# Kernel tuning notes

Measured on AMD Instinct MI355X. Metric: run time of the kernel, lower is better.

## Reference

```python
import jax, jax.numpy as jnp
import numpy as np

B, N, D, H = 8, 4096, 256, 4
KP, KN = N // 16, N // 32
EPS = 1e-6

def _ln(x, g, b):
    m = jnp.mean(x, -1, keepdims=True)
    v = jnp.var(x, -1, keepdims=True)
    return (x - m) / jnp.sqrt(v + 1e-5) * g + b

def _cross_attn(q_in, kv_in, wq, wk, wv, wo, bo):
    # q_in [1,Nq,D], kv_in [1,Nk,D]
    Bq, Nq, Dm = q_in.shape
    Nk = kv_in.shape[1]
    dh = Dm // H
    q = (q_in @ wq).reshape(Bq, Nq, H, dh).transpose(0, 2, 1, 3)
    k = (kv_in @ wk).reshape(Bq, Nk, H, dh).transpose(0, 2, 1, 3)
    v = (kv_in @ wv).reshape(Bq, Nk, H, dh).transpose(0, 2, 1, 3)
    attn = jax.nn.softmax(jnp.einsum('bhqd,bhkd->bhqk', q, k) * (dh ** -0.5), axis=-1)
    out = jnp.einsum('bhqk,bhkd->bhqd', attn, v).transpose(0, 2, 1, 3).reshape(Bq, Nq, Dm)
    return out @ wo + bo

def setup_inputs():
    key = jax.random.key(0)
    ks = jax.random.split(key, 40)
    f32 = jnp.float32
    def w(i, shape, s):
        return s * jax.random.normal(ks[i], shape, f32)
    inp = {}
    inp['x'] = jax.random.normal(ks[0], (B, N, D), f32)
    inp['mask'] = (jax.random.randint(ks[1], (B, N), 0, 3) - 1).astype(jnp.int32)  # values in {-1,0,1}
    inp['pos_emb'] = 0.02 * jax.random.normal(ks[2], (1, N, D), f32)
    inp['sim_p_w'] = w(3, (D, D), 0.2); inp['sim_p_b'] = jnp.zeros((D,), f32)
    inp['sim_n_w'] = w(4, (D, D), 0.2); inp['sim_n_b'] = jnp.zeros((D,), f32)
    inp['adj_w'] = w(5, (D, D), 0.05)
    inp['gnn_p_w1'] = w(6, (D, D), 0.05); inp['gnn_p_w2'] = w(7, (D, D), 0.05)
    inp['gnn_n_w1'] = w(8, (D, D), 0.05); inp['gnn_n_w2'] = w(9, (D, D), 0.05)
    for i in range(1, 6):
        inp['ln%d_g' % i] = jnp.ones((D,), f32)
        inp['ln%d_b' % i] = jnp.zeros((D,), f32)
    names = ['i2q_wq', 'i2q_wk', 'i2q_wv', 'i2q_wo', 'q2i_wq', 'q2i_wk', 'q2i_wv', 'q2i_wo']
    for j, nme in enumerate(names):
        inp[nme] = w(10 + j, (D, D), 0.05)
    inp['i2q_bo'] = jnp.zeros((D,), f32)
    inp['q2i_bo'] = jnp.zeros((D,), f32)
    inp['mlp_w'] = w(20, (D, D), 0.05); inp['mlp_b'] = jnp.zeros((D,), f32)
    inp['g_i2t'] = 0.1 * jax.random.normal(ks[21], (1, 1, D), f32)
    inp['g_t2i'] = 0.1 * jax.random.normal(ks[22], (1, 1, D), f32)
    return inp

def reference(x, mask, pos_emb, sim_p_w, sim_p_b, sim_n_w, sim_n_b, adj_w,
              gnn_p_w1, gnn_p_w2, gnn_n_w1, gnn_n_w2,
              ln1_g, ln1_b, ln2_g, ln2_b, ln3_g, ln3_b, ln4_g, ln4_b, ln5_g, ln5_b,
              i2q_wq, i2q_wk, i2q_wv, i2q_wo, i2q_bo,
              q2i_wq, q2i_wk, q2i_wv, q2i_wo, q2i_bo,
              mlp_w, mlp_b, g_i2t, g_t2i):
    pos_mask = (mask == 1).astype(x.dtype)[..., None]    # [B,N,1]
    neg_mask = (mask == -1).astype(x.dtype)[..., None]
    pos_query = (x * pos_mask).sum(1, keepdims=True) / (pos_mask.sum(1, keepdims=True) + EPS)  # [B,1,D]
    neg_query = (x * neg_mask).sum(1, keepdims=True) / (neg_mask.sum(1, keepdims=True) + EPS)
    pos_sim = jax.nn.sigmoid(((x @ sim_p_w + sim_p_b) * pos_query).sum(-1))  # [B,N]
    neg_sim = jax.nn.sigmoid(((x @ sim_n_w + sim_n_b) * neg_query).sum(-1))
    weight_p, idx_p = jax.lax.top_k(pos_sim, KP)
    weight_n, idx_n = jax.lax.top_k(neg_sim, KN)
    scale = 1.0 / jnp.sqrt(jnp.asarray(D, x.dtype))

    def gcn(node, w1, w2):
        adj = jax.nn.softmax((node @ adj_w) @ node.T * scale, axis=-1)  # [K,K]
        h = jax.nn.relu(adj @ (node @ w1))
        return adj @ (h @ w2)

    def batch_forward(ip, wp, inn, wn, feat):
        node_p = feat[ip] * (wp > 0.6).astype(feat.dtype)[:, None]       # [KP,D]
        query_p = gcn(node_p, gnn_p_w1, gnn_p_w2) + pos_emb[0, ip]
        node_n = feat[inn] * (wn > 0.6).astype(feat.dtype)[:, None]      # [KN,D]
        query_n = gcn(node_n, gnn_n_w1, gnn_n_w2) + pos_emb[0, inn]
        query = jnp.concatenate([query_p, query_n], 0)[None]             # [1,KP+KN,D]
        featb = feat[None]                                               # [1,N,D]
        query = query + g_i2t * _cross_attn(_ln(query, ln1_g, ln1_b), _ln(featb, ln2_g, ln2_b),
                                            i2q_wq, i2q_wk, i2q_wv, i2q_wo, i2q_bo)
        featb = featb + g_t2i * _cross_attn(_ln(featb, ln3_g, ln3_b), _ln(query, ln4_g, ln4_b),
                                            q2i_wq, q2i_wk, q2i_wv, q2i_wo, q2i_bo)
        featb = featb + (_ln(featb, ln5_g, ln5_b) @ mlp_w + mlp_b)
        return featb

    out = jax.vmap(batch_forward)(idx_p, weight_p, idx_n, weight_n, x)   # [B,1,N,D]
    return out, pos_sim, neg_sim
```

## Files before the change

### kernel.cpp

```cpp
#include <hip/hip_runtime.h>

#define BB 8
#define NN 4096
#define DD 256
#define HH 4
#define DHH 64
#define KPP 256
#define KNN 128
#define SCH 64

typedef float f32x4 __attribute__((ext_vector_type(4)));
typedef short bf16x8 __attribute__((ext_vector_type(8)));
typedef short bf16x4 __attribute__((ext_vector_type(4)));

#define FLAG_TRANSB 1
#define FLAG_RELU   2

__device__ __forceinline__ float bf2f(unsigned short u){
  union { unsigned int i; float f; } v; v.i = ((unsigned int)u) << 16; return v.f;
}
__device__ __forceinline__ unsigned short f2bf(float f){
  union { float f; unsigned int i; } v; v.f = f;
  return (unsigned short)((v.i + 0x7FFFu + ((v.i >> 16) & 1u)) >> 16);
}
__device__ __forceinline__ void gload16(const void* g, void* l){
  __builtin_amdgcn_global_load_lds((const __attribute__((address_space(1))) void*)g,
                                   (__attribute__((address_space(3))) void*)l, 16, 0, 0);
}

__global__ __launch_bounds__(256) void stats_part(const float* __restrict__ x,
                                                  const int* __restrict__ mask,
                                                  float* __restrict__ part,
                                                  float* __restrict__ pcnt){
  int b = blockIdx.y, c = blockIdx.x, t = threadIdx.x;
  int w = t >> 6, lane = t & 63;
  const int R = NN / SCH;
  int n0 = c * R;
  const float* xb = x + ((long)b*NN + n0)*DD;
  const int* mb = mask + (long)b*NN + n0;
  float4 sp = {0.f,0.f,0.f,0.f}, sn = {0.f,0.f,0.f,0.f};
  int cp = 0, cn = 0;
  #pragma unroll 4
  for (int r = w; r < R; r += 4){
    int mv = mb[r];
    float4 v = ((const float4*)(xb + (long)r*DD))[lane];
    if (mv == 1){ sp.x += v.x; sp.y += v.y; sp.z += v.z; sp.w += v.w; cp++; }
    else if (mv == -1){ sn.x += v.x; sn.y += v.y; sn.z += v.z; sn.w += v.w; cn++; }
  }
  __shared__ float red[2][4][256];
  __shared__ int cnt[2][4];
  ((float4*)&red[0][w][0])[lane] = sp;
  ((float4*)&red[1][w][0])[lane] = sn;
  if (lane == 0){ cnt[0][w] = cp; cnt[1][w] = cn; }
  __syncthreads();
  float s0 = red[0][0][t]+red[0][1][t]+red[0][2][t]+red[0][3][t];
  float s1 = red[1][0][t]+red[1][1][t]+red[1][2][t]+red[1][3][t];
  part[(((long)(b*SCH+c)*2+0)*DD)+t] = s0;
  part[(((long)(b*SCH+c)*2+1)*DD)+t] = s1;
  if (t == 0){
    pcnt[(b*SCH+c)*2+0] = (float)(cnt[0][0]+cnt[0][1]+cnt[0][2]+cnt[0][3]);
    pcnt[(b*SCH+c)*2+1] = (float)(cnt[1][0]+cnt[1][1]+cnt[1][2]+cnt[1][3]);
  }
}

__global__ void stats_vec(const float* __restrict__ part, const float* __restrict__ pcnt,
                          const float* __restrict__ bp, const float* __restrict__ bn,
                          float* __restrict__ qpn, float* __restrict__ cscal){
  int b = blockIdx.x, k = threadIdx.x;
  __shared__ float red[256];
  float sp=0.f, sn=0.f, cp=0.f, cn=0.f;
  for (int c = 0; c < SCH; c++){
    sp += part[(((long)(b*SCH+c)*2+0)*DD)+k];
    sn += part[(((long)(b*SCH+c)*2+1)*DD)+k];
    cp += pcnt[(b*SCH+c)*2+0];
    cn += pcnt[(b*SCH+c)*2+1];
  }
  float qpv = sp / (cp + 1e-6f);
  float qnv = sn / (cn + 1e-6f);
  qpn[(long)(b*2+0)*DD + k] = qpv;
  qpn[(long)(b*2+1)*DD + k] = qnv;
  red[k] = bp[k]*qpv;
  __syncthreads();
  for (int s = 128; s > 0; s >>= 1){ if (k < s) red[k] += red[k+s]; __syncthreads(); }
  if (k == 0) cscal[b*2+0] = red[0];
  __syncthreads();
  red[k] = bn[k]*qnv;
  __syncthreads();
  for (int s = 128; s > 0; s >>= 1){ if (k < s) red[k] += red[k+s]; __syncthreads(); }
  if (k == 0) cscal[b*2+1] = red[0];
}

__global__ void simvec_par(const float* __restrict__ qpn,
                           const float* __restrict__ Wp, const float* __restrict__ Wn,
                           float* __restrict__ vvec){
  int c = blockIdx.x, b = blockIdx.y, t = threadIdx.x;
  __shared__ float qp[256], qn[256];
  qp[t] = qpn[(long)(b*2+0)*DD + t];
  qn[t] = qpn[(long)(b*2+1)*DD + t];
  __syncthreads();
  int row = c*32 + (t >> 3);
  int seg = (t & 7)*32;
  const float* wp = Wp + (long)row*DD + seg;
  const float* wn = Wn + (long)row*DD + seg;
  float ap = 0.f, an = 0.f;
  #pragma unroll 8
  for (int j = 0; j < 32; j++){ ap += wp[j]*qp[seg+j]; an += wn[j]*qn[seg+j]; }
  #pragma unroll
  for (int off = 1; off < 8; off <<= 1){ ap += __shfl_xor(ap, off); an += __shfl_xor(an, off); }
  if ((t & 7) == 0){
    vvec[(long)(b*2+0)*DD + row] = ap;
    vvec[(long)(b*2+1)*DD + row] = an;
  }
}

__global__ void sim_norm_kernel(const float* __restrict__ x, const float* __restrict__ vvec,
                                const float* __restrict__ cscal,
                                float* __restrict__ simP, float* __restrict__ simN,
                                unsigned short* __restrict__ xhat){
  int b = blockIdx.y;
  int w = threadIdx.x >> 6, lane = threadIdx.x & 63;
  int n = blockIdx.x*4 + w;
  long row = (long)b*NN + n;
  const float4* xr = (const float4*)(x + row*DD);
  float4 xv = xr[lane];
  float4 a = ((const float4*)(vvec + (long)(b*2+0)*DD))[lane];
  float4 c = ((const float4*)(vvec + (long)(b*2+1)*DD))[lane];
  float sp = xv.x*a.x + xv.y*a.y + xv.z*a.z + xv.w*a.w;
  float sn = xv.x*c.x + xv.y*c.y + xv.z*c.z + xv.w*c.w;
  float s  = xv.x+xv.y+xv.z+xv.w;
  float q  = xv.x*xv.x+xv.y*xv.y+xv.z*xv.z+xv.w*xv.w;
  for (int off = 32; off; off >>= 1){
    sp += __shfl_xor(sp, off); sn += __shfl_xor(sn, off);
    s  += __shfl_xor(s, off);  q  += __shfl_xor(q, off);
  }
  float m = s*(1.f/256.f);
  float var = q*(1.f/256.f) - m*m;
  float rinv = rsqrtf(var + 1e-5f);
  ushort4 o;
  o.x = f2bf((xv.x-m)*rinv); o.y = f2bf((xv.y-m)*rinv);
  o.z = f2bf((xv.z-m)*rinv); o.w = f2bf((xv.w-m)*rinv);
  ((ushort4*)(xhat + row*DD))[lane] = o;
  if (lane == 0){
    float zp = sp + cscal[b*2+0], zn = sn + cscal[b*2+1];
    simP[row] = 1.f/(1.f+expf(-zp));
    simN[row] = 1.f/(1.f+expf(-zn));
  }
}

__global__ __launch_bounds__(256) void topk_radix(const float* __restrict__ simP,
                                                  const float* __restrict__ simN,
                                                  const float* __restrict__ x,
                                                  int* __restrict__ idxb, float* __restrict__ wb,
                                                  float* __restrict__ node){
  __shared__ unsigned int vals[4096];
  __shared__ unsigned int hist[4096];
  __shared__ unsigned short eql[4096];
  __shared__ unsigned int tsum[256];
  __shared__ unsigned int sB, sRem, sCG, sCnt, sEq;
  int id = blockIdx.x; int sgn = id & 1, b = id >> 1;
  int K = (sgn == 0) ? KPP : KNN;
  const float* s = (sgn == 0 ? simP : simN) + (long)b*NN;
  int t = threadIdx.x;
  if (t == 0){ sCG = 0; sCnt = 0; sEq = 0; }
  for (int i = t; i < 4096; i += 256){ vals[i] = __float_as_uint(s[i]); hist[i] = 0; }
  __syncthreads();

  auto find_thresh = [&](int NB, unsigned need){
    int per = NB >> 8;
    int base = t*per;
    unsigned local = 0;
    for (int j = 0; j < per; j++) local += hist[base+j];
    tsum[t] = local;
    __syncthreads();
    #pragma unroll
    for (int st = 1; st < 256; st <<= 1){
      unsigned v = (t + st < 256) ? tsum[t+st] : 0u;
      __syncthreads();
      tsum[t] += v;
      __syncthreads();
    }
    unsigned after = (t < 255) ? tsum[t+1] : 0u;
    if (after < need && after + local >= need){
      unsigned c = after;
      for (int j = per-1; j >= 0; j--){
        unsigned h = hist[base+j];
        c += h;
        if (c >= need){
          sB = (unsigned)(base+j);
          sRem = need - (c - h);
          atomicAdd(&sCG, c - h);
          break;
        }
      }
    }
    __syncthreads();
  };

  for (int i = t; i < 4096; i += 256) atomicAdd(&hist[vals[i] >> 20], 1u);
  __syncthreads();
  find_thresh(4096, (unsigned)K);
  unsigned B1 = sB, rem1 = sRem;
  __syncthreads();
  for (int i = t; i < 4096; i += 256) hist[i] = 0;
  __syncthreads();
  for (int i = t; i < 4096; i += 256){
    unsigned v = vals[i];
    if ((v >> 20) == B1) atomicAdd(&hist[(v >> 8) & 0xFFFu], 1u);
  }
  __syncthreads();
  find_thresh(4096, rem1);
  unsigned B2 = sB, rem2 = sRem;
  unsigned pre = (B1 << 12) | B2;
  __syncthreads();
  hist[t] = 0;
  __syncthreads();
  for (int i = t; i < 4096; i += 256){
    unsigned v = vals[i];
    if ((v >> 8) == pre) atomicAdd(&hist[v & 0xFFu], 1u);
  }
  __syncthreads();
  find_thresh(256, rem2);
  unsigned T = (pre << 8) | sB;
  unsigned cg = sCG;
  __syncthreads();
  hist[t] = 0;
  __syncthreads();

  int* oi = idxb + (long)id*256;
  float* ow = wb + (long)id*256;
  for (int i = t; i < 4096; i += 256){
    unsigned v = vals[i];
    if (v > T){
      unsigned p = atomicAdd(&sCnt, 1u);
      oi[p] = i; ow[p] = __uint_as_float(v);
      hist[p] = (unsigned)i; hist[256+p] = v;
    }
    else if (v == T){ unsigned e = atomicAdd(&sEq, 1u); eql[e] = (unsigned short)i; }
  }
  __syncthreads();
  int ne = K - (int)cg;
  int eqn = (int)sEq;
  for (int e = t; e < eqn; e += 256){
    int myi = eql[e]; int r = 0;
    for (int e2 = 0; e2 < eqn; e2++) r += (eql[e2] < myi);
    if (r < ne){
      oi[cg + r] = myi; ow[cg + r] = __uint_as_float(T);
      hist[cg + r] = (unsigned)myi; hist[256 + cg + r] = T;
    }
  }
  __syncthreads();
  int rbase = (sgn == 0) ? 0 : KPP;
  int lane = t & 63, rw = t >> 6;
  for (int i0 = 0; i0 < K; i0 += 4){
    int r = i0 + rw;
    int idx = (int)hist[r];
    float wv = __uint_as_float(hist[256 + r]);
    float4 vsel;
    if (wv > 0.6f) vsel = ((const float4*)(x + ((long)b*NN + idx)*DD))[lane];
    else vsel = (float4){0.f,0.f,0.f,0.f};
    ((float4*)(node + ((long)b*384 + rbase + r)*DD))[lane] = vsel;
  }
}

__global__ void softmax_dual(float* __restrict__ A0, int L0, int rpb0, long bs0, int rows0,
                             float* __restrict__ A1, int L1, int rpb1, long bs1, int rows1){
  int w = threadIdx.x >> 6, lane = threadIdx.x & 63;
  long row = (long)blockIdx.x*4 + w;
  float* A; int L, rpb; long bs;
  if (row < rows0){ A = A0; L = L0; rpb = rpb0; bs = bs0; }
  else { row -= rows0; if (row >= rows1) return; A = A1; L = L1; rpb = rpb1; bs = bs1; }
  int b = (int)(row / rpb), r = (int)(row % rpb);
  float* a = A + (long)b*bs + (long)r*L;
  int e = L >> 6;
  float vals[4]; float mx = -1e30f;
  for (int j = 0; j < e; j++){ vals[j] = a[lane*e+j]; mx = fmaxf(mx, vals[j]); }
  for (int off = 32; off; off >>= 1) mx = fmaxf(mx, __shfl_xor(mx, off));
  float sum = 0.f;
  for (int j = 0; j < e; j++){ vals[j] = expf(vals[j]-mx); sum += vals[j]; }
  for (int off = 32; off; off >>= 1) sum += __shfl_xor(sum, off);
  float rinv = 1.f/sum;
  for (int j = 0; j < e; j++) a[lane*e+j] = vals[j]*rinv;
}

__global__ void rownorm_kernel(const float* __restrict__ X, unsigned short* __restrict__ Y, int rows){
  int w = threadIdx.x >> 6, lane = threadIdx.x & 63;
  long row = (long)blockIdx.x*4 + w;
  if (row >= rows) return;
  const float4* xr = (const float4*)(X + row*DD);
  float4 xv = xr[lane];
  float s = xv.x+xv.y+xv.z+xv.w;
  float q = xv.x*xv.x+xv.y*xv.y+xv.z*xv.z+xv.w*xv.w;
  for (int off = 32; off; off >>= 1){ s += __shfl_xor(s, off); q += __shfl_xor(q, off); }
  float m = s*(1.f/256.f);
  float var = q*(1.f/256.f) - m*m;
  float rinv = rsqrtf(var + 1e-5f);
  ushort4 o;
  o.x = f2bf((xv.x-m)*rinv); o.y = f2bf((xv.y-m)*rinv);
  o.z = f2bf((xv.z-m)*rinv); o.w = f2bf((xv.w-m)*rinv);
  ((ushort4*)(Y + row*DD))[lane] = o;
}

struct FoldArgs { const float* W[9]; const float* g[9]; unsigned short* BT[9]; float sc[9]; };
struct BiasArgs { const float* W[7]; const float* b[7]; const float* addb[7]; float* out[7]; float sc[7]; };

__global__ void fold_all(FoldArgs fa, BiasArgs ba){
  __shared__ float T[64][65];
  int t = threadIdx.x;
  if (blockIdx.y < 9){
    int m = blockIdx.y, tile = blockIdx.x;
    const float* W = fa.W[m]; const float* g = fa.g[m]; unsigned short* BT = fa.BT[m];
    float sc = fa.sc[m];
    int tn = (tile & 3)*64, tk = (tile >> 2)*64;
    #pragma unroll 4
    for (int p = 0; p < 16; p++){
      int kl = p*4 + (t >> 6), nl = t & 63;
      float v = W[(long)(tk+kl)*256 + tn + nl];
      if (g) v *= g[tk+kl];
      T[kl][nl] = v * sc;
    }
    __syncthreads();
    #pragma unroll 4
    for (int p = 0; p < 16; p++){
      int nl = p*4 + (t >> 6), kl = t & 63;
      BT[(long)(tn+nl)*256 + tk + kl] = f2bf(T[kl][nl]);
    }
  } else if (blockIdx.x < 7){
    int m = blockIdx.x, n = t;
    const float* W = ba.W[m]; const float* b = ba.b[m];
    float s = (ba.addb[m] != nullptr) ? ba.addb[m][n] : 0.f;
    for (int k = 0; k < 256; k++) s += b[k]*W[(long)k*256+n];
    ba.out[m][n] = s * ba.sc[m];
  }
}

struct GP {
  const float* A; long sAb; int lda;
  const float* B; long sBb; int ldb;
  float* C; long sCb; int ldc;
  const int* pidx; const float* pe;
  int M, N, K; float alpha; int flags;
};
struct GP4 { GP p[4]; };

__global__ __launch_bounds__(256) void gemm_multi(GP4 g4){
  GP p = g4.p[blockIdx.z >> 3];
  int b = blockIdx.z & 7;
  int m0 = blockIdx.y*64, n0 = blockIdx.x*64;
  if (m0 >= p.M || n0 >= p.N) return;
  __shared__ __align__(16) unsigned short As[64*40];
  __shared__ __align__(16) unsigned short Bs[64*40];
  const float* Ab = p.A + (long)b*p.sAb;
  const float* Bb = p.B + (long)b*p.sBb;
  int t = threadIdx.x;
  int w = t >> 6, lane = t & 63, lrowi = lane & 15, lquad = lane >> 4;
  int wm = w >> 1, wn = w & 1;
  f32x4 acc[2][2];
  #pragma unroll
  for (int i = 0; i < 2; i++)
    #pragma unroll
    for (int j = 0; j < 2; j++) acc[i][j] = (f32x4){0.f,0.f,0.f,0.f};
  int am = t >> 2, akq = t & 3;
  for (int k0 = 0; k0 < p.K; k0 += 32){
    {
      const float4* s4 = (const float4*)(Ab + (long)(m0+am)*p.lda + k0 + akq*8);
      float4 u = s4[0], vv = s4[1];
      unsigned short tmp[8];
      tmp[0]=f2bf(u.x); tmp[1]=f2bf(u.y); tmp[2]=f2bf(u.z); tmp[3]=f2bf(u.w);
      tmp[4]=f2bf(vv.x); tmp[5]=f2bf(vv.y); tmp[6]=f2bf(vv.z); tmp[7]=f2bf(vv.w);
      *(uint4*)(&As[am*40 + akq*8]) = *(uint4*)tmp;
    }
    if (p.flags & FLAG_TRANSB){
      const float4* s4 = (const float4*)(Bb + (long)(n0+am)*p.ldb + k0 + akq*8);
      float4 u = s4[0], vv = s4[1];
      unsigned short tmp[8];
      tmp[0]=f2bf(u.x); tmp[1]=f2bf(u.y); tmp[2]=f2bf(u.z); tmp[3]=f2bf(u.w);
      tmp[4]=f2bf(vv.x); tmp[5]=f2bf(vv.y); tmp[6]=f2bf(vv.z); tmp[7]=f2bf(vv.w);
      *(uint4*)(&Bs[am*40 + akq*8]) = *(uint4*)tmp;
    } else {
      int bn = t & 63, bkb = (t >> 6)*8;
      #pragma unroll
      for (int j = 0; j < 8; j++)
        Bs[bn*40 + bkb + j] = f2bf(Bb[(long)(k0+bkb+j)*p.ldb + n0 + bn]);
    }
    __syncthreads();
    bf16x8 af[2], bfr[2];
    #pragma unroll
    for (int i = 0; i < 2; i++)
      af[i] = *(const bf16x8*)(&As[(wm*32 + i*16 + lrowi)*40 + lquad*8]);
    #pragma unroll
    for (int j = 0; j < 2; j++)
      bfr[j] = *(const bf16x8*)(&Bs[(wn*32 + j*16 + lrowi)*40 + lquad*8]);
    #pragma unroll
    for (int i = 0; i < 2; i++)
      #pragma unroll
      for (int j = 0; j < 2; j++)
        acc[i][j] = __builtin_amdgcn_mfma_f32_16x16x32_bf16(af[i], bfr[j], acc[i][j], 0, 0, 0);
    __syncthreads();
  }
  float* Cb = p.C + (long)b*p.sCb;
  #pragma unroll
  for (int i = 0; i < 2; i++)
    #pragma unroll
    for (int j = 0; j < 2; j++){
      int col = n0 + wn*32 + j*16 + lrowi;
      #pragma unroll
      for (int r = 0; r < 4; r++){
        int row = m0 + wm*32 + i*16 + lquad*4 + r;
        float v = p.alpha*acc[i][j][r];
        if (p.flags & FLAG_RELU) v = fmaxf(v, 0.f);
        if (p.pidx != nullptr){
          int idx = p.pidx[b*512 + row];
          v += p.pe[(long)idx*256 + col];
        }
        Cb[(long)row*p.ldc + col] = v;
      }
    }
}

template<typename OT, bool RES, bool GATE>
__device__ __forceinline__ void gemm128_body(
    const unsigned short* __restrict__ A, long sAb,
    const unsigned short* __restrict__ BT,
    OT* __restrict__ C, long sCb, int ldc,
    const float* __restrict__ R, long sRb,
    const float* __restrict__ bias, const float* __restrict__ gate,
    int bx, int by, int bz,
    unsigned short (&As)[2][4096], unsigned short (&Bs)[2][4096])
{
  int t = threadIdx.x;
  int w = t >> 6, lane = t & 63, lrowi = lane & 15, lquad = lane >> 4;
  int wm = w >> 1, wn = w & 1;
  int m0 = by*128, n0 = bx*128;
  const unsigned short* Ab = A + (long)bz*sAb + (long)m0*256;
  const unsigned short* Bb = BT + (long)n0*256;
  int g0 = t, g1 = 256 + t;
  int row0 = g0 >> 2, kq0 = g0 & 3;
  int row1 = g1 >> 2, kq1 = g1 & 3;
  f32x4 acc[4][4];
  #pragma unroll
  for (int i = 0; i < 4; i++)
    #pragma unroll
    for (int j = 0; j < 4; j++) acc[i][j] = (f32x4){0.f,0.f,0.f,0.f};

  auto stage = [&](int buf, int k0){
    gload16(Ab + (long)row0*256 + k0 + kq0*8, &As[buf][g0*8]);
    gload16(Ab + (long)row1*256 + k0 + kq1*8, &As[buf][g1*8]);
    gload16(Bb + (long)row0*256 + k0 + kq0*8, &Bs[buf][g0*8]);
    gload16(Bb + (long)row1*256 + k0 + kq1*8, &Bs[buf][g1*8]);
  };

  stage(0, 0);
  for (int it = 0; it < 8; it++){
    int cur = it & 1;
    if (it < 7){
      stage(cur ^ 1, (it+1)*32);
      __asm__ volatile("s_waitcnt vmcnt(4)" ::: "memory");
    } else {
      __asm__ volatile("s_waitcnt vmcnt(0)" ::: "memory");
    }
    __builtin_amdgcn_s_barrier();
    bf16x8 af[4], bfr[4];
    #pragma unroll
    for (int i = 0; i < 4; i++)
      af[i] = *(const bf16x8*)(&As[cur][((wm*64 + i*16 + lrowi)*4 + lquad)*8]);
    #pragma unroll
    for (int j = 0; j < 4; j++)
      bfr[j] = *(const bf16x8*)(&Bs[cur][((wn*64 + j*16 + lrowi)*4 + lquad)*8]);
    #pragma unroll
    for (int i = 0; i < 4; i++)
      #pragma unroll
      for (int j = 0; j < 4; j++)
        acc[i][j] = __builtin_amdgcn_mfma_f32_16x16x32_bf16(af[i], bfr[j], acc[i][j], 0, 0, 0);
    __asm__ volatile("s_waitcnt lgkmcnt(0)" ::: "memory");
    __builtin_amdgcn_s_barrier();
  }
  OT* Cb = C + (long)bz*sCb;
  const float* Rb = RES ? (R + (long)bz*sRb) : nullptr;
  #pragma unroll
  for (int j = 0; j < 4; j++){
    int col = n0 + wn*64 + j*16 + lrowi;
    float bv = bias[col];
    float gv = GATE ? gate[col] : 1.f;
    #pragma unroll
    for (int i = 0; i < 4; i++){
      #pragma unroll
      for (int r = 0; r < 4; r++){
        int row = m0 + wm*64 + i*16 + lquad*4 + r;
        float v = acc[i][j][r] + bv;
        if (GATE) v *= gv;
        if (RES) v += Rb[(long)row*256 + col];
        if constexpr (sizeof(OT) == 4) Cb[(long)row*ldc + col] = v;
        else                           Cb[(long)row*ldc + col] = f2bf(v);
      }
    }
  }
}

template<typename OT, bool RES, bool GATE>
__global__ __launch_bounds__(256) void gemm128(
    const unsigned short* __restrict__ A, long sAb,
    const unsigned short* __restrict__ BT,
    OT* __restrict__ C, long sCb, int ldc,
    const float* __restrict__ R, long sRb,
    const float* __restrict__ bias, const float* __restrict__ gate)
{
  __shared__ __align__(16) unsigned short As[2][4096];
  __shared__ __align__(16) unsigned short Bs[2][4096];
  gemm128_body<OT,RES,GATE>(A, sAb, BT, C, sCb, ldc, R, sRb, bias, gate,
                            blockIdx.x, blockIdx.y, blockIdx.z, As, Bs);
}

__global__ __launch_bounds__(256) void gemm128_pair(
    const unsigned short* __restrict__ A0, long sA0, const unsigned short* __restrict__ B0,
    unsigned short* __restrict__ C0, long sC0, int ldc0, const float* __restrict__ bias0,
    const unsigned short* __restrict__ A1, long sA1, const unsigned short* __restrict__ B1,
    unsigned short* __restrict__ C1, long sC1, int ldc1, const float* __restrict__ bias1)
{
  __shared__ __align__(16) unsigned short As[2][4096];
  __shared__ __align__(16) unsigned short Bs[2][4096];
  int x = blockIdx.x, z = blockIdx.z;
  if (x < 192){
    gemm128_body<unsigned short,false,false>(A0, sA0, B0, C0, sC0, ldc0, nullptr, 0, bias0, nullptr,
                                             x % 6, x / 6, z, As, Bs);
  } else {
    int xx = x - 192;
    gemm128_body<unsigned short,false,false>(A1, sA1, B1, C1, sC1, ldc1, nullptr, 0, bias1, nullptr,
                                             xx % 2, xx / 2, z, As, Bs);
  }
}

template<int NFRAG>
__global__ __launch_bounds__(256) void flash_kernel(
    const unsigned short* __restrict__ Q, long sQb, int ldq,
    const unsigned short* __restrict__ Kt, const unsigned short* __restrict__ Vt,
    long sKb, int ldkv,
    unsigned short* __restrict__ O, long sOb,
    float* __restrict__ Opart, float* __restrict__ Lpart,
    int Nq, int Nk, int nsplit)
{
  __shared__ __align__(16) unsigned short Kl[2][32*72];
  __shared__ __align__(16) unsigned short Vl[2][64*36];
  __shared__ __align__(16) unsigned short Pl[4*NFRAG*16*36];
  int b = blockIdx.z, h = blockIdx.y;
  int nqg = Nq / (64*NFRAG);
  int qg = blockIdx.x % nqg, split = blockIdx.x / nqg;
  int kchunk = Nk / nsplit;
  int kbeg = split*kchunk, kend = kbeg + kchunk;
  int t = threadIdx.x, w = t >> 6, lane = t & 63, lrowi = lane & 15, lquad = lane >> 4;
  int q0 = qg*(64*NFRAG) + w*(16*NFRAG);
  const unsigned short* Qb = Q + (long)b*sQb + h*DHH;
  const unsigned short* Kb = Kt + (long)b*sKb + h*DHH;
  const unsigned short* Vb = Vt + (long)b*sKb + h*DHH;
  bf16x8 qa[NFRAG][2];
  #pragma unroll
  for (int f = 0; f < NFRAG; f++)
    #pragma unroll
    for (int kt = 0; kt < 2; kt++)
      qa[f][kt] = *(const bf16x8*)(Qb + (long)(q0 + f*16 + lrowi)*ldq + kt*32 + lquad*8);

  f32x4 o[NFRAG][4];
  float psum[NFRAG][4];
  #pragma unroll
  for (int f = 0; f < NFRAG; f++)
    #pragma unroll
    for (int cj = 0; cj < 4; cj++){
      o[f][cj] = (f32x4){0.f,0.f,0.f,0.f};
      psum[f][cj] = 0.f;
    }
  int skq = t >> 3, sdq = (t & 7)*8;
  int skrow = ((skq & 1) << 4) | (skq >> 1);
  int vkq = t & 31, vdq = (t >> 5)*8;
  unsigned short* Pw = &Pl[w*(NFRAG*16*36)];

  for (int kt0 = kbeg; kt0 < kend; kt0 += 64){
    {
      uint4 k0v = *(const uint4*)(Kb + (long)(kt0+skq)*ldkv + sdq);
      uint4 v0v = *(const uint4*)(Vb + (long)(kt0+vkq)*ldkv + vdq);
      uint4 k1v = *(const uint4*)(Kb + (long)(kt0+32+skq)*ldkv + sdq);
      uint4 v1v = *(const uint4*)(Vb + (long)(kt0+32+vkq)*ldkv + vdq);
      *(uint4*)(&Kl[0][skrow*72 + sdq]) = k0v;
      const unsigned short* vp0 = (const unsigned short*)&v0v;
      #pragma unroll
      for (int j = 0; j < 8; j++) Vl[0][(vdq+j)*36 + vkq] = vp0[j];
      *(uint4*)(&Kl[1][skrow*72 + sdq]) = k1v;
      const unsigned short* vp1 = (const unsigned short*)&v1v;
      #pragma unroll
      for (int j = 0; j < 8; j++) Vl[1][(vdq+j)*36 + vkq] = vp1[j];
    }
    __syncthreads();
    #pragma unroll
    for (int s = 0; s < 2; s++){
      bf16x8 kb0 = *(const bf16x8*)(&Kl[s][(0*16+lrowi)*72 + lquad*8]);
      bf16x8 kb1 = *(const bf16x8*)(&Kl[s][(0*16+lrowi)*72 + 32 + lquad*8]);
      bf16x8 kb2 = *(const bf16x8*)(&Kl[s][(1*16+lrowi)*72 + lquad*8]);
      bf16x8 kb3 = *(const bf16x8*)(&Kl[s][(1*16+lrowi)*72 + 32 + lquad*8]);
      union { bf16x8 v8; bf16x4 v4[2]; } vbu[4];
      #pragma unroll
      for (int cj = 0; cj < 4; cj++){
        const unsigned short* vb = &Vl[s][(cj*16+lrowi)*36 + lquad*8];
        vbu[cj].v4[0] = *(const bf16x4*)vb;
        vbu[cj].v4[1] = *(const bf16x4*)(vb + 4);
      }
      #pragma unroll
      for (int f = 0; f < NFRAG; f++){
        f32x4 S0 = (f32x4){0.f,0.f,0.f,0.f}, S1 = (f32x4){0.f,0.f,0.f,0.f};
        __builtin_amdgcn_s_setprio(1);
        S0 = __builtin_amdgcn_mfma_f32_16x16x32_bf16(qa[f][0], kb0, S0, 0, 0, 0);
        S0 = __builtin_amdgcn_mfma_f32_16x16x32_bf16(qa[f][1], kb1, S0, 0, 0, 0);
        S1 = __builtin_amdgcn_mfma_f32_16x16x32_bf16(qa[f][0], kb2, S1, 0, 0, 0);
        S1 = __builtin_amdgcn_mfma_f32_16x16x32_bf16(qa[f][1], kb3, S1, 0, 0, 0);
        __builtin_amdgcn_s_setprio(0);
        unsigned short* Pf = Pw + f*(16*36);
        #pragma unroll
        for (int r = 0; r < 4; r++){
          float p0 = exp2f(S0[r]);
          float p1 = exp2f(S1[r]);
          psum[f][r] += p0 + p1;
          unsigned int pk;
          asm("v_cvt_pk_bf16_f32 %0, %1, %2" : "=v"(pk) : "v"(p0), "v"(p1));
          *(unsigned int*)(&Pf[(lquad*4+r)*36 + 2*lrowi]) = pk;
        }
      }
      __asm__ volatile("s_waitcnt lgkmcnt(0)" ::: "memory");
      #pragma unroll
      for (int f = 0; f < NFRAG; f++){
        const unsigned short* pp = &Pw[f*(16*36) + lrowi*36 + lquad*8];
        union { bf16x8 v8; bf16x4 v4[2]; } pa;
        pa.v4[0] = *(const bf16x4*)pp;
        pa.v4[1] = *(const bf16x4*)(pp + 4);
        __builtin_amdgcn_s_setprio(1);
        #pragma unroll
        for (int cj = 0; cj < 4; cj++)
          o[f][cj] = __builtin_amdgcn_mfma_f32_16x16x32_bf16(pa.v8, vbu[cj].v8, o[f][cj], 0, 0, 0);
        __builtin_amdgcn_s_setprio(0);
      }
    }
    __syncthreads();
  }
  float lsum[NFRAG][4];
  #pragma unroll
  for (int f = 0; f < NFRAG; f++)
    #pragma unroll
    for (int r = 0; r < 4; r++){
      float s = psum[f][r];
      #pragma unroll
      for (int off = 1; off < 16; off <<= 1) s += __shfl_xor(s, off);
      lsum[f][r] = s;
    }
  if (nsplit > 1){
    int p = (b*HH + h)*nsplit + split;
    float* Op = Opart + (long)p*Nq*DHH;
    #pragma unroll
    for (int f = 0; f < NFRAG; f++)
      #pragma unroll
      for (int r = 0; r < 4; r++){
        int row = q0 + f*16 + lquad*4 + r;
        #pragma unroll
        for (int cj = 0; cj < 4; cj++)
          Op[(long)row*DHH + cj*16 + lrowi] = o[f][cj][r];
        if (lrowi == 0) Lpart[(long)p*Nq + row] = lsum[f][r];
      }
  } else {
    unsigned short* Ob = O + (long)b*sOb + h*DHH;
    #pragma unroll
    for (int f = 0; f < NFRAG; f++)
      #pragma unroll
      for (int r = 0; r < 4; r++){
        float rl = 1.f/lsum[f][r];
        int row = q0 + f*16 + lquad*4 + r;
        #pragma unroll
        for (int cj = 0; cj < 4; cj++)
          Ob[(long)row*DD + cj*16 + lrowi] = f2bf(o[f][cj][r]*rl);
      }
  }
}

__global__ void flash_combine(const float* __restrict__ Opart, const float* __restrict__ Lpart,
                              unsigned short* __restrict__ O, long sOb, int Nq, int nsplit){
  int gr = blockIdx.x*4 + (threadIdx.x >> 6);
  int d = threadIdx.x & 63;
  int bh = gr / Nq, row = gr % Nq;
  float accO = 0.f, accL = 0.f;
  for (int s = 0; s < nsplit; s++){
    long p = (long)bh*nsplit + s;
    accL += Lpart[p*Nq + row];
    accO += Opart[(p*Nq + row)*DHH + d];
  }
  int b = bh / HH, h = bh % HH;
  O[(long)b*sOb + (long)row*DD + h*DHH + d] = f2bf(accO/accL);
}

extern "C" void kernel_launch(void* const* d_in, const int* in_sizes, int n_in,
                              void* d_out, int out_size, void* d_ws, size_t ws_size,
                              hipStream_t stream) {
  (void)in_sizes; (void)n_in; (void)out_size; (void)ws_size;
  const float* x        = (const float*)d_in[0];
  const int*   mask     = (const int*)d_in[1];
  const float* pos_emb  = (const float*)d_in[2];
  const float* sim_p_w  = (const float*)d_in[3];
  const float* sim_p_b  = (const float*)d_in[4];
  const float* sim_n_w  = (const float*)d_in[5];
  const float* sim_n_b  = (const float*)d_in[6];
  const float* adj_w    = (const float*)d_in[7];
  const float* gnn_p_w1 = (const float*)d_in[8];
  const float* gnn_p_w2 = (const float*)d_in[9];
  const float* gnn_n_w1 = (const float*)d_in[10];
  const float* gnn_n_w2 = (const float*)d_in[11];
  const float* ln1_g = (const float*)d_in[12]; const float* ln1_b = (const float*)d_in[13];
  const float* ln2_g = (const float*)d_in[14]; const float* ln2_b = (const float*)d_in[15];
  const float* ln3_g = (const float*)d_in[16]; const float* ln3_b = (const float*)d_in[17];
  const float* ln4_g = (const float*)d_in[18]; const float* ln4_b = (const float*)d_in[19];
  const float* ln5_g = (const float*)d_in[20]; const float* ln5_b = (const float*)d_in[21];
  const float* i2q_wq = (const float*)d_in[22];
  const float* i2q_wk = (const float*)d_in[23];
  const float* i2q_wv = (const float*)d_in[24];
  const float* i2q_wo = (const float*)d_in[25];
  const float* q2i_wq = (const float*)d_in[26];
  const float* q2i_wk = (const float*)d_in[27];
  const float* q2i_wv = (const float*)d_in[28];
  const float* q2i_wo = (const float*)d_in[29];
  const float* i2q_bo = (const float*)d_in[30];
  const float* q2i_bo = (const float*)d_in[31];
  const float* mlp_w  = (const float*)d_in[32];
  const float* mlp_b  = (const float*)d_in[33];
  const float* g_i2t  = (const float*)d_in[34];
  const float* g_t2i  = (const float*)d_in[35];

  float* out  = (float*)d_out;
  float* simP = out + (size_t)BB*NN*DD;
  float* simN = simP + (size_t)BB*NN;

  char* w8 = (char*)d_ws;
  size_t off = 0;
  auto take = [&](size_t bytes)->void*{
    void* p = (void*)(w8 + off);
    off += (bytes + 255) & ~(size_t)255;
    return p;
  };
  float* part   = (float*)take((size_t)BB*SCH*2*DD*4);
  float* pcnt   = (float*)take((size_t)BB*SCH*2*4);
  float* vvec   = (float*)take((size_t)BB*2*DD*4);
  float* qpn    = (float*)take((size_t)BB*2*DD*4);
  float* cscal  = (float*)take((size_t)BB*2*4);
  int*   idxb   = (int*)take((size_t)BB*2*256*4);
  float* wb     = (float*)take((size_t)BB*2*256*4);
  float* node   = (float*)take((size_t)BB*384*DD*4);
  float* gA     = (float*)take((size_t)BB*384*DD*4);
  float* gadjP  = (float*)take((size_t)BB*256*256*4);
  float* gadjN  = (float*)take((size_t)BB*128*128*4);
  float* query  = (float*)take((size_t)BB*384*DD*4);
  float* query2 = (float*)take((size_t)BB*384*DD*4);
  unsigned short* xhatq  = (unsigned short*)take((size_t)BB*384*DD*2);
  unsigned short* qh     = (unsigned short*)take((size_t)BB*384*DD*2);
  unsigned short* attnZ  = (unsigned short*)take((size_t)BB*384*DD*2);
  unsigned short* xhatq2 = (unsigned short*)take((size_t)BB*384*DD*2);
  unsigned short* kv2    = (unsigned short*)take((size_t)BB*384*512*2);
  unsigned short* xhat   = (unsigned short*)take((size_t)BB*NN*DD*2);
  unsigned short* kvq    = (unsigned short*)take((size_t)BB*NN*768*2);
  float* featb2 = (float*)take((size_t)BB*NN*DD*4);
  float* Lpart  = (float*)take((size_t)BB*HH*8*384*4);
  unsigned short* wTq1  = (unsigned short*)take((size_t)65536*2);
  unsigned short* wTbig = (unsigned short*)take((size_t)3*65536*2);
  unsigned short* wTkv2 = (unsigned short*)take((size_t)2*65536*2);
  unsigned short* wTmlp = (unsigned short*)take((size_t)65536*2);
  unsigned short* wTo1  = (unsigned short*)take((size_t)65536*2);
  unsigned short* wTo2  = (unsigned short*)take((size_t)65536*2);
  float* biasQ1  = (float*)take(256*4);
  float* biasBig = (float*)take(768*4);
  float* biasKV2 = (float*)take(512*4);
  float* biasMlp = (float*)take(256*4);
  float* t1 = query;
  float* t2 = query2;
  float* t3 = gA;
  unsigned short* attn2 = xhat;
  unsigned short* xhat5 = kvq;
  float* Opart = featb2;

  const long sQ  = 384L*DD;
  const long sX  = (long)NN*DD;
  const float* NF = nullptr;

  const float QS = 0.125f * 1.44269504088896f;

  FoldArgs fa;
  fa.W[0]=i2q_wq; fa.g[0]=ln1_g; fa.BT[0]=wTq1;            fa.sc[0]=QS;
  fa.W[1]=i2q_wk; fa.g[1]=ln2_g; fa.BT[1]=wTbig;           fa.sc[1]=1.f;
  fa.W[2]=i2q_wv; fa.g[2]=ln2_g; fa.BT[2]=wTbig + 256*256; fa.sc[2]=1.f;
  fa.W[3]=q2i_wq; fa.g[3]=ln3_g; fa.BT[3]=wTbig + 512*256; fa.sc[3]=QS;
  fa.W[4]=q2i_wk; fa.g[4]=ln4_g; fa.BT[4]=wTkv2;           fa.sc[4]=1.f;
  fa.W[5]=q2i_wv; fa.g[5]=ln4_g; fa.BT[5]=wTkv2 + 256*256; fa.sc[5]=1.f;
  fa.W[6]=mlp_w;  fa.g[6]=ln5_g; fa.BT[6]=wTmlp;           fa.sc[6]=1.f;
  fa.W[7]=i2q_wo; fa.g[7]=nullptr; fa.BT[7]=wTo1;          fa.sc[7]=1.f;
  fa.W[8]=q2i_wo; fa.g[8]=nullptr; fa.BT[8]=wTo2;          fa.sc[8]=1.f;
  BiasArgs ba;
  ba.W[0]=i2q_wq; ba.b[0]=ln1_b; ba.addb[0]=nullptr; ba.out[0]=biasQ1;     ba.sc[0]=QS;
  ba.W[1]=i2q_wk; ba.b[1]=ln2_b; ba.addb[1]=nullptr; ba.out[1]=biasBig;    ba.sc[1]=1.f;
  ba.W[2]=i2q_wv; ba.b[2]=ln2_b; ba.addb[2]=nullptr; ba.out[2]=biasBig+256; ba.sc[2]=1.f;
  ba.W[3]=q2i_wq; ba.b[3]=ln3_b; ba.addb[3]=nullptr; ba.out[3]=biasBig+512; ba.sc[3]=QS;
  ba.W[4]=q2i_wk; ba.b[4]=ln4_b; ba.addb[4]=nullptr; ba.out[4]=biasKV2;    ba.sc[4]=1.f;
  ba.W[5]=q2i_wv; ba.b[5]=ln4_b; ba.addb[5]=nullptr; ba.out[5]=biasKV2+256; ba.sc[5]=1.f;
  ba.W[6]=mlp_w;  ba.b[6]=ln5_b; ba.addb[6]=mlp_b;   ba.out[6]=biasMlp;    ba.sc[6]=1.f;
  fold_all<<<dim3(16,10), 256, 0, stream>>>(fa, ba);

  stats_part<<<dim3(SCH, BB), 256, 0, stream>>>(x, mask, part, pcnt);
  stats_vec<<<BB, 256, 0, stream>>>(part, pcnt, sim_p_b, sim_n_b, qpn, cscal);
  simvec_par<<<dim3(8, BB), 256, 0, stream>>>(qpn, sim_p_w, sim_n_w, vvec);
  sim_norm_kernel<<<dim3(NN/4, BB), 256, 0, stream>>>(x, vvec, cscal, simP, simN, xhat);
  topk_radix<<<2*BB, 256, 0, stream>>>(simP, simN, x, idxb, wb, node);

  GP z = {};
  {
    GP4 g;
    g.p[0] = { node, 384L*DD, 256, adj_w, 0, 256, gA, 384L*DD, 256, nullptr, nullptr, 384, 256, 256, 1.f, 0 };
    g.p[1] = { node, 384L*DD, 256, gnn_p_w1, 0, 256, t1, 384L*DD, 256, nullptr, nullptr, 256, 256, 256, 1.f, 0 };
    g.p[2] = { node + 256L*DD, 384L*DD, 256, gnn_n_w1, 0, 256, t1 + 256L*DD, 384L*DD, 256, nullptr, nullptr, 128, 256, 256, 1.f, 0 };
    g.p[3] = z;
    gemm_multi<<<dim3(4,6,3*BB), 256, 0, stream>>>(g);
  }
  {
    GP4 g;
    g.p[0] = { gA, 384L*DD, 256, node, 384L*DD, 256, gadjP, 65536L, 256, nullptr, nullptr, 256, 256, 256, 0.0625f, FLAG_TRANSB };
    g.p[1] = { gA + 256L*DD, 384L*DD, 256, node + 256L*DD, 384L*DD, 256, gadjN, 16384L, 128, nullptr, nullptr, 128, 128, 256, 0.0625f, FLAG_TRANSB };
    g.p[2] = z; g.p[3] = z;
    gemm_multi<<<dim3(4,4,2*BB), 256, 0, stream>>>(g);
  }
  softmax_dual<<<768, 256, 0, stream>>>(gadjP, 256, 256, 65536L, BB*256,
                                        gadjN, 128, 128, 16384L, BB*128);
  {
    GP4 g;
    g.p[0] = { gadjP, 65536L, 256, t1, 384L*DD, 256, t2, 384L*DD, 256, nullptr, nullptr, 256, 256, 256, 1.f, FLAG_RELU };
    g.p[1] = { gadjN, 16384L, 128, t1 + 256L*DD, 384L*DD, 256, t2 + 256L*DD, 384L*DD, 256, nullptr, nullptr, 128, 256, 128, 1.f, FLAG_RELU };
    g.p[2] = z; g.p[3] = z;
    gemm_multi<<<dim3(4,4,2*BB), 256, 0, stream>>>(g);
  }
  {
    GP4 g;
    g.p[0] = { t2, 384L*DD, 256, gnn_p_w2, 0, 256, t3, 384L*DD, 256, nullptr, nullptr, 256, 256, 256, 1.f, 0 };
    g.p[1] = { t2 + 256L*DD, 384L*DD, 256, gnn_n_w2, 0, 256, t3 + 256L*DD, 384L*DD, 256, nullptr, nullptr, 128, 256, 256, 1.f, 0 };
    g.p[2] = z; g.p[3] = z;
    gemm_multi<<<dim3(4,4,2*BB), 256, 0, stream>>>(g);
  }
  {
    GP4 g;
    g.p[0] = { gadjP, 65536L, 256, t3, 384L*DD, 256, query, 384L*DD, 256, idxb, pos_emb, 256, 256, 256, 1.f, 0 };
    g.p[1] = { gadjN, 16384L, 128, t3 + 256L*DD, 384L*DD, 256, query + 256L*DD, 384L*DD, 256, idxb + 256, pos_emb, 128, 256, 128, 1.f, 0 };
    g.p[2] = z; g.p[3] = z;
    gemm_multi<<<dim3(4,4,2*BB), 256, 0, stream>>>(g);
  }

  rownorm_kernel<<<BB*384/4, 256, 0, stream>>>(query, xhatq, BB*384);

  gemm128_pair<<<dim3(198,1,BB),256,0,stream>>>(
      xhat, sX, wTbig, kvq, (long)NN*768, 768, biasBig,
      xhatq, sQ, wTq1, qh, sQ, 256, biasQ1);
  flash_kernel<3><<<dim3(2*8, HH, BB), 256, 0, stream>>>(
      qh, sQ, 256, kvq, kvq + 256, (long)NN*768, 768,
      attnZ, sQ, Opart, Lpart, 384, NN, 8);
  flash_combine<<<BB*HH*384/4, 256, 0, stream>>>(Opart, Lpart, attnZ, sQ, 384, 8);
  gemm128<float,true,true><<<dim3(2,3,BB),256,0,stream>>>(
      attnZ, sQ, wTo1, query2, sQ, 256, query, sQ, i2q_bo, g_i2t);

  rownorm_kernel<<<BB*384/4, 256, 0, stream>>>(query2, xhatq2, BB*384);
  gemm128<unsigned short,false,false><<<dim3(4,3,BB),256,0,stream>>>(
      xhatq2, sQ, wTkv2, kv2, 384L*512, 512, NF, 0, biasKV2, NF);
  flash_kernel<2><<<dim3(32, HH, BB), 256, 0, stream>>>(
      kvq + 512, (long)NN*768, 768, kv2, kv2 + 256, 384L*512, 512,
      attn2, sX, nullptr, nullptr, NN, 384, 1);
  gemm128<float,true,true><<<dim3(2,32,BB),256,0,stream>>>(
      attn2, sX, wTo2, featb2, sX, 256, x, sX, q2i_bo, g_t2i);

  rownorm_kernel<<<BB*NN/4, 256, 0, stream>>>(featb2, xhat5, BB*NN);
  gemm128<float,true,false><<<dim3(2,32,BB),256,0,stream>>>(
      xhat5, sX, wTmlp, out, sX, 256, featb2, sX, biasMlp, NF);
}
```

Before: 456.0 us.

## Fuse GCN GEMM chain and softmax into one cooperative kernel with grid syncs

Replaces five gemm_multi launches plus the softmax launch with a single cooperative kernel of 576 blocks that runs each stage in turn, separated by grid-wide barriers. The aim is to remove per-launch overhead and the idle gaps between the small dependent GCN stages. In exchange, later stages use only 256 of the 576 blocks, and grid.sync itself adds cost. The cooperative launch also requires all 576 blocks to be resident at once.

```diff
diff --git a/kernel.cpp b/kernel.cpp
--- a/kernel.cpp
+++ b/kernel.cpp
@@ -1,4 +1,7 @@
 #include <hip/hip_runtime.h>
+#include <hip/hip_cooperative_groups.h>
+
+namespace cg = cooperative_groups;
 
 #define BB 8
 #define NN 4096
@@ -221,7 +224,7 @@
   __syncthreads();
   find_thresh(256, rem2);
   unsigned T = (pre << 8) | sB;
-  unsigned cg = sCG;
+  unsigned cg2 = sCG;
   __syncthreads();
   hist[t] = 0;
   __syncthreads();
@@ -238,14 +241,14 @@
     else if (v == T){ unsigned e = atomicAdd(&sEq, 1u); eql[e] = (unsigned short)i; }
   }
   __syncthreads();
-  int ne = K - (int)cg;
+  int ne = K - (int)cg2;
   int eqn = (int)sEq;
   for (int e = t; e < eqn; e += 256){
     int myi = eql[e]; int r = 0;
     for (int e2 = 0; e2 < eqn; e2++) r += (eql[e2] < myi);
     if (r < ne){
-      oi[cg + r] = myi; ow[cg + r] = __uint_as_float(T);
-      hist[cg + r] = (unsigned)myi; hist[256 + cg + r] = T;
+      oi[cg2 + r] = myi; ow[cg2 + r] = __uint_as_float(T);
+      hist[cg2 + r] = (unsigned)myi; hist[256 + cg2 + r] = T;
     }
   }
   __syncthreads();
@@ -260,26 +263,6 @@
     else vsel = (float4){0.f,0.f,0.f,0.f};
     ((float4*)(node + ((long)b*384 + rbase + r)*DD))[lane] = vsel;
   }
-}
-
-__global__ void softmax_dual(float* __restrict__ A0, int L0, int rpb0, long bs0, int rows0,
-                             float* __restrict__ A1, int L1, int rpb1, long bs1, int rows1){
-  int w = threadIdx.x >> 6, lane = threadIdx.x & 63;
-  long row = (long)blockIdx.x*4 + w;
-  float* A; int L, rpb; long bs;
-  if (row < rows0){ A = A0; L = L0; rpb = rpb0; bs = bs0; }
-  else { row -= rows0; if (row >= rows1) return; A = A1; L = L1; rpb = rpb1; bs = bs1; }
-  int b = (int)(row / rpb), r = (int)(row % rpb);
-  float* a = A + (long)b*bs + (long)r*L;
-  int e = L >> 6;
-  float vals[4]; float mx = -1e30f;
-  for (int j = 0; j < e; j++){ vals[j] = a[lane*e+j]; mx = fmaxf(mx, vals[j]); }
-  for (int off = 32; off; off >>= 1) mx = fmaxf(mx, __shfl_xor(mx, off));
-  float sum = 0.f;
-  for (int j = 0; j < e; j++){ vals[j] = expf(vals[j]-mx); sum += vals[j]; }
-  for (int off = 32; off; off >>= 1) sum += __shfl_xor(sum, off);
-  float rinv = 1.f/sum;
-  for (int j = 0; j < e; j++) a[lane*e+j] = vals[j]*rinv;
 }
 
 __global__ void rownorm_kernel(const float* __restrict__ X, unsigned short* __restrict__ Y, int rows){
@@ -340,15 +323,11 @@
   const int* pidx; const float* pe;
   int M, N, K; float alpha; int flags;
 };
-struct GP4 { GP p[4]; };
-
-__global__ __launch_bounds__(256) void gemm_multi(GP4 g4){
-  GP p = g4.p[blockIdx.z >> 3];
-  int b = blockIdx.z & 7;
-  int m0 = blockIdx.y*64, n0 = blockIdx.x*64;
+
+__device__ __forceinline__ void gemm64(const GP& p, int bx, int by, int b,
+                                       unsigned short* As, unsigned short* Bs){
+  int m0 = by*64, n0 = bx*64;
   if (m0 >= p.M || n0 >= p.N) return;
-  __shared__ __align__(16) unsigned short As[64*40];
-  __shared__ __align__(16) unsigned short Bs[64*40];
   const float* Ab = p.A + (long)b*p.sAb;
   const float* Bb = p.B + (long)b*p.sBb;
   int t = threadIdx.x;
@@ -415,6 +394,51 @@
         Cb[(long)row*p.ldc + col] = v;
       }
     }
+}
+
+__device__ __forceinline__ void softmax_v(float* A0, int L0, int rpb0, long bs0, int rows0,
+                                          float* A1, int L1, int rpb1, long bs1, int rows1,
+                                          int vb){
+  int w = threadIdx.x >> 6, lane = threadIdx.x & 63;
+  long row = (long)vb*4 + w;
+  float* A; int L, rpb; long bs;
+  if (row < rows0){ A = A0; L = L0; rpb = rpb0; bs = bs0; }
+  else { row -= rows0; if (row >= rows1) return; A = A1; L = L1; rpb = rpb1; bs = bs1; }
+  int b = (int)(row / rpb), r = (int)(row % rpb);
+  float* a = A + (long)b*bs + (long)r*L;
+  int e = L >> 6;
+  float vals[4]; float mx = -1e30f;
+  for (int j = 0; j < e; j++){ vals[j] = a[lane*e+j]; mx = fmaxf(mx, vals[j]); }
+  for (int off = 32; off; off >>= 1) mx = fmaxf(mx, __shfl_xor(mx, off));
+  float sum = 0.f;
+  for (int j = 0; j < e; j++){ vals[j] = expf(vals[j]-mx); sum += vals[j]; }
+  for (int off = 32; off; off >>= 1) sum += __shfl_xor(sum, off);
+  float rinv = 1.f/sum;
+  for (int j = 0; j < e; j++) a[lane*e+j] = vals[j]*rinv;
+}
+
+struct GcnArgs {
+  GP p1[3]; GP p2[2]; GP p4[2]; GP p5[2]; GP p6[2];
+  float* A0; float* A1;
+};
+
+__global__ __launch_bounds__(256) void gcn_fused(GcnArgs ga){
+  __shared__ __align__(16) unsigned short As[64*40];
+  __shared__ __align__(16) unsigned short Bs[64*40];
+  cg::grid_group grid = cg::this_grid();
+  int id = blockIdx.x;
+  { int bz = id/24, r = id - bz*24; gemm64(ga.p1[bz>>3], r&3, r>>2, bz&7, As, Bs); }
+  grid.sync();
+  if (id < 256){ int bz = id>>4; gemm64(ga.p2[bz>>3], id&3, (id>>2)&3, bz&7, As, Bs); }
+  grid.sync();
+  for (int vb = id; vb < 768; vb += 576)
+    softmax_v(ga.A0, 256, 256, 65536L, BB*256, ga.A1, 128, 128, 16384L, BB*128, vb);
+  grid.sync();
+  if (id < 256){ int bz = id>>4; gemm64(ga.p4[bz>>3], id&3, (id>>2)&3, bz&7, As, Bs); }
+  grid.sync();
+  if (id < 256){ int bz = id>>4; gemm64(ga.p5[bz>>3], id&3, (id>>2)&3, bz&7, As, Bs); }
+  grid.sync();
+  if (id < 256){ int bz = id>>4; gemm64(ga.p6[bz>>3], id&3, (id>>2)&3, bz&7, As, Bs); }
 }
 
 template<typename OT, bool RES, bool GATE>
@@ -808,44 +832,22 @@
   sim_norm_kernel<<<dim3(NN/4, BB), 256, 0, stream>>>(x, vvec, cscal, simP, simN, xhat);
   topk_radix<<<2*BB, 256, 0, stream>>>(simP, simN, x, idxb, wb, node);
 
-  GP z = {};
+  GcnArgs ga;
+  ga.p1[0] = { node, 384L*DD, 256, adj_w, 0, 256, gA, 384L*DD, 256, nullptr, nullptr, 384, 256, 256, 1.f, 0 };
+  ga.p1[1] = { node, 384L*DD, 256, gnn_p_w1, 0, 256, t1, 384L*DD, 256, nullptr, nullptr, 256, 256, 256, 1.f, 0 };
+  ga.p1[2] = { node + 256L*DD, 384L*DD, 256, gnn_n_w1, 0, 256, t1 + 256L*DD, 384L*DD, 256, nullptr, nullptr, 128, 256, 256, 1.f, 0 };
+  ga.p2[0] = { gA, 384L*DD, 256, node, 384L*DD, 256, gadjP, 65536L, 256, nullptr, nullptr, 256, 256, 256, 0.0625f, FLAG_TRANSB };
+  ga.p2[1] = { gA + 256L*DD, 384L*DD, 256, node + 256L*DD, 384L*DD, 256, gadjN, 16384L, 128, nullptr, nullptr, 128, 128, 256, 0.0625f, FLAG_TRANSB };
+  ga.p4[0] = { gadjP, 65536L, 256, t1, 384L*DD, 256, t2, 384L*DD, 256, nullptr, nullptr, 256, 256, 256, 1.f, FLAG_RELU };
+  ga.p4[1] = { gadjN, 16384L, 128, t1 + 256L*DD, 384L*DD, 256, t2 + 256L*DD, 384L*DD, 256, nullptr, nullptr, 128, 256, 128, 1.f, FLAG_RELU };
+  ga.p5[0] = { t2, 384L*DD, 256, gnn_p_w2, 0, 256, t3, 384L*DD, 256, nullptr, nullptr, 256, 256, 256, 1.f, 0 };
+  ga.p5[1] = { t2 + 256L*DD, 384L*DD, 256, gnn_n_w2, 0, 256, t3 + 256L*DD, 384L*DD, 256, nullptr, nullptr, 128, 256, 256, 1.f, 0 };
+  ga.p6[0] = { gadjP, 65536L, 256, t3, 384L*DD, 256, query, 384L*DD, 256, idxb, pos_emb, 256, 256, 256, 1.f, 0 };
+  ga.p6[1] = { gadjN, 16384L, 128, t3 + 256L*DD, 384L*DD, 256, query + 256L*DD, 384L*DD, 256, idxb + 256, pos_emb, 128, 256, 128, 1.f, 0 };
+  ga.A0 = gadjP; ga.A1 = gadjN;
   {
-    GP4 g;
-    g.p[0] = { node, 384L*DD, 256, adj_w, 0, 256, gA, 384L*DD, 256, nullptr, nullptr, 384, 256, 256, 1.f, 0 };
-    g.p[1] = { node, 384L*DD, 256, gnn_p_w1, 0, 256, t1, 384L*DD, 256, nullptr, nullptr, 256, 256, 256, 1.f, 0 };
-    g.p[2] = { node + 256L*DD, 384L*DD, 256, gnn_n_w1, 0, 256, t1 + 256L*DD, 384L*DD, 256, nullptr, nullptr, 128, 256, 256, 1.f, 0 };
-    g.p[3] = z;
-    gemm_multi<<<dim3(4,6,3*BB), 256, 0, stream>>>(g);
-  }
-  {
-    GP4 g;
-    g.p[0] = { gA, 384L*DD, 256, node, 384L*DD, 256, gadjP, 65536L, 256, nullptr, nullptr, 256, 256, 256, 0.0625f, FLAG_TRANSB };
-    g.p[1] = { gA + 256L*DD, 384L*DD, 256, node + 256L*DD, 384L*DD, 256, gadjN, 16384L, 128, nullptr, nullptr, 128, 128, 256, 0.0625f, FLAG_TRANSB };
-    g.p[2] = z; g.p[3] = z;
-    gemm_multi<<<dim3(4,4,2*BB), 256, 0, stream>>>(g);
-  }
-  softmax_dual<<<768, 256, 0, stream>>>(gadjP, 256, 256, 65536L, BB*256,
-                                        gadjN, 128, 128, 16384L, BB*128);
-  {
-    GP4 g;
-    g.p[0] = { gadjP, 65536L, 256, t1, 384L*DD, 256, t2, 384L*DD, 256, nullptr, nullptr, 256, 256, 256, 1.f, FLAG_RELU };
-    g.p[1] = { gadjN, 16384L, 128, t1 + 256L*DD, 384L*DD, 256, t2 + 256L*DD, 384L*DD, 256, nullptr, nullptr, 128, 256, 128, 1.f, FLAG_RELU };
-    g.p[2] = z; g.p[3] = z;
-    gemm_multi<<<dim3(4,4,2*BB), 256, 0, stream>>>(g);
-  }
-  {
-    GP4 g;
-    g.p[0] = { t2, 384L*DD, 256, gnn_p_w2, 0, 256, t3, 384L*DD, 256, nullptr, nullptr, 256, 256, 256, 1.f, 0 };
-    g.p[1] = { t2 + 256L*DD, 384L*DD, 256, gnn_n_w2, 0, 256, t3 + 256L*DD, 384L*DD, 256, nullptr, nullptr, 128, 256, 256, 1.f, 0 };
-    g.p[2] = z; g.p[3] = z;
-    gemm_multi<<<dim3(4,4,2*BB), 256, 0, stream>>>(g);
-  }
-  {
-    GP4 g;
-    g.p[0] = { gadjP, 65536L, 256, t3, 384L*DD, 256, query, 384L*DD, 256, idxb, pos_emb, 256, 256, 256, 1.f, 0 };
-    g.p[1] = { gadjN, 16384L, 128, t3 + 256L*DD, 384L*DD, 256, query + 256L*DD, 384L*DD, 256, idxb + 256, pos_emb, 128, 256, 128, 1.f, 0 };
-    g.p[2] = z; g.p[3] = z;
-    gemm_multi<<<dim3(4,4,2*BB), 256, 0, stream>>>(g);
+    void* kp[] = { (void*)&ga };
+    hipLaunchCooperativeKernel((void*)gcn_fused, dim3(576), dim3(256), kp, 0, stream);
   }
 
   rownorm_kernel<<<BB*384/4, 256, 0, stream>>>(query, xhatq, BB*384);
```

Measured after the change: 848.1 us. +86.0%, slower.
